# Optimization experiments

Hardware: AMD Instinct MI355X
Metric: run time of the kernel (lower is better)

## Reference

```python
import jax, jax.numpy as jnp
import numpy as np

EPS = 1e-8  # matches torch cosine_similarity eps


def setup_inputs() -> dict:
    key = jax.random.key(0)
    k1, k2 = jax.random.split(key)
    B, D = 8192, 128
    hid_positive = jax.random.normal(k1, (B, D), dtype=jnp.float32)
    hid_anchor = jax.random.normal(k2, (B, D), dtype=jnp.float32)
    return {"hid_positive": hid_positive, "hid_anchor": hid_anchor}


def reference(hid_positive, hid_anchor):
    # Original: anchor_batch = repeat_interleave(anchor, B) pairs every anchor i
    # with every positive j (positive[i] first per block, then the rest).
    # idx = +1 exactly on the (i, i) pairs, -1 elsewhere.
    # CosineEmbeddingLoss(margin=0, reduction='mean'):
    #   y=+1: 1 - cos ;  y=-1: max(0, cos)
    # Equivalent fused form: pairwise cosine matrix + masked loss, mean over B*B.
    a = hid_anchor / jnp.maximum(
        jnp.linalg.norm(hid_anchor, axis=1, keepdims=True), EPS)
    p = hid_positive / jnp.maximum(
        jnp.linalg.norm(hid_positive, axis=1, keepdims=True), EPS)
    cos = a @ p.T  # [B, B]; cos[i, j] = cos(anchor_i, positive_j)
    B = cos.shape[0]
    diag = jnp.eye(B, dtype=bool)
    loss = jnp.where(diag, 1.0 - cos, jnp.maximum(cos, 0.0))
    return jnp.mean(loss)
```

## Files before the change

### kernel.cpp

```cpp
#include <hip/hip_runtime.h>

typedef float f32x4 __attribute__((ext_vector_type(4)));
typedef int   i32x4 __attribute__((ext_vector_type(4)));
typedef int   i32x8 __attribute__((ext_vector_type(8)));

#define D 128
#define NBLK 256

__global__ void normalize_diag_kernel(const float* __restrict__ anc,
                                      const float* __restrict__ pos,
                                      unsigned char* __restrict__ wsA,
                                      unsigned char* __restrict__ wsP,
                                      float* __restrict__ diagP,
                                      int* __restrict__ counter) {
  if (blockIdx.x == 0 && threadIdx.x == 0)
    __hip_atomic_store(counter, 0, __ATOMIC_RELAXED, __HIP_MEMORY_SCOPE_AGENT);
  __shared__ float rowc[16];
  const int t = threadIdx.x;
  const int rl = t >> 4, l16 = t & 15;
  const int row = blockIdx.x * 16 + rl;
  const float* ar = anc + (size_t)row * D + l16 * 8;
  const float* pr = pos + (size_t)row * D + l16 * 8;
  float4 a0 = *(const float4*)ar, a1 = *(const float4*)(ar + 4);
  float4 p0 = *(const float4*)pr, p1 = *(const float4*)(pr + 4);
  float av[8] = {a0.x, a0.y, a0.z, a0.w, a1.x, a1.y, a1.z, a1.w};
  float pv[8] = {p0.x, p0.y, p0.z, p0.w, p1.x, p1.y, p1.z, p1.w};
  float ssa = 0.f, ssp = 0.f;
#pragma unroll
  for (int k = 0; k < 8; ++k) { ssa += av[k] * av[k]; ssp += pv[k] * pv[k]; }
#pragma unroll
  for (int off = 1; off < 16; off <<= 1) {
    ssa += __shfl_xor(ssa, off);
    ssp += __shfl_xor(ssp, off);
  }
  const float sa = 1.f / fmaxf(sqrtf(ssa), 1e-8f);
  const float sp = 1.f / fmaxf(sqrtf(ssp), 1e-8f);
  float an[8], pn[8];
  float dot = 0.f;
#pragma unroll
  for (int k = 0; k < 8; ++k) {
    an[k] = av[k] * sa;
    pn[k] = pv[k] * sp;
    dot += an[k] * pn[k];
  }
  int wa0 = __builtin_amdgcn_cvt_pk_fp8_f32(an[0], an[1], 0, false);
  wa0 = __builtin_amdgcn_cvt_pk_fp8_f32(an[2], an[3], wa0, true);
  int wa1 = __builtin_amdgcn_cvt_pk_fp8_f32(an[4], an[5], 0, false);
  wa1 = __builtin_amdgcn_cvt_pk_fp8_f32(an[6], an[7], wa1, true);
  int wp0 = __builtin_amdgcn_cvt_pk_fp8_f32(pn[0], pn[1], 0, false);
  wp0 = __builtin_amdgcn_cvt_pk_fp8_f32(pn[2], pn[3], wp0, true);
  int wp1 = __builtin_amdgcn_cvt_pk_fp8_f32(pn[4], pn[5], 0, false);
  wp1 = __builtin_amdgcn_cvt_pk_fp8_f32(pn[6], pn[7], wp1, true);
  *(int2*)(wsA + (size_t)row * D + l16 * 8) = make_int2(wa0, wa1);
  *(int2*)(wsP + (size_t)row * D + l16 * 8) = make_int2(wp0, wp1);
#pragma unroll
  for (int off = 1; off < 16; off <<= 1) dot += __shfl_xor(dot, off);
  if (l16 == 0) rowc[rl] = 1.f - dot - fmaxf(dot, 0.f);
  __syncthreads();
  if (t == 0) {
    float s = 0.f;
#pragma unroll
    for (int i = 0; i < 16; ++i) s += rowc[i];
    diagP[blockIdx.x] = s;
  }
}

__global__ __launch_bounds__(512, 2) void gemm_relu_sum_kernel(
    const unsigned char* __restrict__ wsA,
    const unsigned char* __restrict__ wsP,
    float* __restrict__ partials, const float* __restrict__ diagP,
    int* __restrict__ counter, float* __restrict__ out, float invBB) {
  __shared__ __align__(16) unsigned char ldsA[256 * 128];
  __shared__ __align__(16) unsigned char ldsB[4][128 * 128];
  __shared__ float wpart[8];
  __shared__ int lastFlag;
  const int tid = threadIdx.x;
  const int bid = blockIdx.x;
  const int w = tid >> 6, l = tid & 63;
  const int r16 = l & 15, kg = l >> 4;
  const int wrow = w >> 2, wcol = w & 3;
  const int rp = bid >> 3;
  const int cg = bid & 7;

  const unsigned char* gA = wsA + (size_t)rp * 256 * D;
  const unsigned char* gB = wsP + (size_t)(cg * 1024) * D;

#define STAGE_B(buf, tile)                                                     \
  {                                                                            \
    const unsigned char* gBt = gB + (size_t)(tile) * 128 * D;                  \
    char* lB = (char*)ldsB[buf];                                               \
    _Pragma("unroll") for (int it = 0; it < 2; ++it) {                         \
      const int g = it * 512 + tid;                                            \
      const int r = g >> 3, sl = g & 7;                                        \
      const int goff = r * 128 + ((sl ^ (r & 7)) * 16);                        \
      const int lbase = (it * 512 + w * 64) * 16;                              \
      __builtin_amdgcn_global_load_lds(                                        \
          (const __attribute__((address_space(1))) char*)(gBt + goff),         \
          (__attribute__((address_space(3))) char*)(lB + lbase), 16, 0, 0);    \
    }                                                                          \
  }

#pragma unroll
  for (int it = 0; it < 4; ++it) {
    const int g = it * 512 + tid;
    const int r = g >> 3, sl = g & 7;
    const int goff = r * 128 + ((sl ^ (r & 7)) * 16);
    const int lbase = (it * 512 + w * 64) * 16;
    __builtin_amdgcn_global_load_lds(
        (const __attribute__((address_space(1))) char*)(gA + goff),
        (__attribute__((address_space(3))) char*)((char*)ldsA + lbase), 16, 0, 0);
  }
  STAGE_B(0, 0)
  STAGE_B(1, 1)

  asm volatile("s_waitcnt vmcnt(4)" ::: "memory");
  __builtin_amdgcn_s_barrier();

  i32x8 af[8];
#pragma unroll
  for (int m = 0; m < 8; ++m) {
    const int r = wrow * 128 + m * 16 + r16;
    const unsigned char* base = (const unsigned char*)ldsA + r * 128;
    i32x4 lo = *(const i32x4*)(base + (((2 * kg) ^ (r & 7)) * 16));
    i32x4 hi = *(const i32x4*)(base + (((2 * kg + 1) ^ (r & 7)) * 16));
    af[m] = __builtin_shufflevector(lo, hi, 0, 1, 2, 3, 4, 5, 6, 7);
  }

  float s0 = 0.f, s1 = 0.f, s2 = 0.f, s3 = 0.f;
#pragma unroll
  for (int t = 0; t < 8; ++t) {
    if (t < 6) STAGE_B((t + 2) & 3, t + 2)
    if (t < 6)      asm volatile("s_waitcnt vmcnt(4)" ::: "memory");
    else if (t == 6) asm volatile("s_waitcnt vmcnt(2)" ::: "memory");
    else             asm volatile("s_waitcnt vmcnt(0)" ::: "memory");
    __builtin_amdgcn_s_barrier();

    const unsigned char* lB = (const unsigned char*)ldsB[t & 3];
    i32x8 bfr[2];
#pragma unroll
    for (int n = 0; n < 2; ++n) {
      const int r = wcol * 32 + n * 16 + r16;
      const unsigned char* base = lB + r * 128;
      i32x4 lo = *(const i32x4*)(base + (((2 * kg) ^ (r & 7)) * 16));
      i32x4 hi = *(const i32x4*)(base + (((2 * kg + 1) ^ (r & 7)) * 16));
      bfr[n] = __builtin_shufflevector(lo, hi, 0, 1, 2, 3, 4, 5, 6, 7);
    }

    f32x4 acc[8][2] = {};
    __builtin_amdgcn_s_setprio(1);
#pragma unroll
    for (int m = 0; m < 8; ++m)
#pragma unroll
      for (int n = 0; n < 2; ++n)
        acc[m][n] = __builtin_amdgcn_mfma_scale_f32_16x16x128_f8f6f4(
            af[m], bfr[n], acc[m][n], 0, 0,
            0, 0x7f7f7f7f, 0, 0x7f7f7f7f);
    __builtin_amdgcn_s_setprio(0);

#pragma unroll
    for (int m = 0; m < 8; ++m)
#pragma unroll
      for (int n = 0; n < 2; ++n) {
        s0 += fmaxf(acc[m][n][0], 0.f);
        s1 += fmaxf(acc[m][n][1], 0.f);
        s2 += fmaxf(acc[m][n][2], 0.f);
        s3 += fmaxf(acc[m][n][3], 0.f);
      }
  }

  float s = (s0 + s1) + (s2 + s3);
#pragma unroll
  for (int off = 32; off >= 1; off >>= 1) s += __shfl_xor(s, off);
  if (l == 0) wpart[w] = s;
  __syncthreads();
  if (tid == 0) {
    float b = 0.f;
#pragma unroll
    for (int i = 0; i < 8; ++i) b += wpart[i];
    __hip_atomic_store(&partials[bid], b, __ATOMIC_RELAXED,
                       __HIP_MEMORY_SCOPE_AGENT);
    __threadfence();
    const int ticket = __hip_atomic_fetch_add(counter, 1, __ATOMIC_ACQ_REL,
                                              __HIP_MEMORY_SCOPE_AGENT);
    lastFlag = (ticket == NBLK - 1) ? 1 : 0;
  }
  __syncthreads();

  if (lastFlag) {
    __threadfence();
    float v = diagP[tid];
    if (tid < NBLK)
      v += __hip_atomic_load(&partials[tid], __ATOMIC_RELAXED,
                             __HIP_MEMORY_SCOPE_AGENT);
#pragma unroll
    for (int off = 32; off >= 1; off >>= 1) v += __shfl_xor(v, off);
    if (l == 0) wpart[w] = v;
    __syncthreads();
    if (tid == 0) {
      float tot = 0.f;
#pragma unroll
      for (int i = 0; i < 8; ++i) tot += wpart[i];
      out[0] = tot * invBB;
    }
  }
#undef STAGE_B
}

extern "C" void kernel_launch(void* const* d_in, const int* in_sizes, int n_in,
                              void* d_out, int out_size, void* d_ws, size_t ws_size,
                              hipStream_t stream) {
  const float* pos = (const float*)d_in[0];
  const float* anc = (const float*)d_in[1];
  const int B = in_sizes[0] / D;

  char* ws = (char*)d_ws;
  unsigned char* wsA = (unsigned char*)ws;
  unsigned char* wsP = (unsigned char*)(ws + (size_t)B * D);
  float* partials = (float*)(ws + (size_t)2 * B * D);
  float* diagP = partials + NBLK;
  int* counter = (int*)(diagP + 512);

  const int nDiag = B / 16;
  const float invBB = 1.0f / ((float)B * (float)B);

  normalize_diag_kernel<<<nDiag, 256, 0, stream>>>(anc, pos, wsA, wsP, diagP,
                                                   counter);
  gemm_relu_sum_kernel<<<NBLK, 512, 0, stream>>>(wsA, wsP, partials, diagP,
                                                 counter, (float*)d_out, invBB);
}
```

Measured before the change: 31.39 us.

## Replace pipelined B-tile loop with one 256x128 tile per block over 2048 blocks

The GEMM kernel used 256 blocks of 512 threads, each looping over eight 128-column B tiles with a 4-deep global_load_lds pipeline. It now launches 2048 blocks of 256 threads, each computing a single 256x128 output tile with no inner loop, and raises occupancy to 3 blocks per CU. This removes the pipeline and barrier logic and spreads work over more blocks. In exchange, the A tile is reloaded 8x more often and each block stalls on its loads with no overlap. The final reduction now covers 2048 partials.

```diff
diff --git a/kernel.cpp b/kernel.cpp
--- a/kernel.cpp
+++ b/kernel.cpp
@@ -5,7 +5,7 @@
 typedef int   i32x8 __attribute__((ext_vector_type(8)));
 
 #define D 128
-#define NBLK 256
+#define GBLK 2048
 
 __global__ void normalize_diag_kernel(const float* __restrict__ anc,
                                       const float* __restrict__ pos,
@@ -65,56 +65,46 @@
   }
 }
 
-__global__ __launch_bounds__(512, 2) void gemm_relu_sum_kernel(
+__global__ __launch_bounds__(256, 3) void gemm_relu_sum_kernel(
     const unsigned char* __restrict__ wsA,
     const unsigned char* __restrict__ wsP,
     float* __restrict__ partials, const float* __restrict__ diagP,
     int* __restrict__ counter, float* __restrict__ out, float invBB) {
   __shared__ __align__(16) unsigned char ldsA[256 * 128];
-  __shared__ __align__(16) unsigned char ldsB[4][128 * 128];
-  __shared__ float wpart[8];
+  __shared__ __align__(16) unsigned char ldsB[128 * 128];
+  __shared__ float wpart[4];
   __shared__ int lastFlag;
   const int tid = threadIdx.x;
   const int bid = blockIdx.x;
   const int w = tid >> 6, l = tid & 63;
   const int r16 = l & 15, kg = l >> 4;
-  const int wrow = w >> 2, wcol = w & 3;
-  const int rp = bid >> 3;
-  const int cg = bid & 7;
+  const int wrow = w >> 1, wcol = w & 1;
+  const int rp = bid >> 6;
+  const int ct = bid & 63;
 
   const unsigned char* gA = wsA + (size_t)rp * 256 * D;
-  const unsigned char* gB = wsP + (size_t)(cg * 1024) * D;
-
-#define STAGE_B(buf, tile)                                                     \
-  {                                                                            \
-    const unsigned char* gBt = gB + (size_t)(tile) * 128 * D;                  \
-    char* lB = (char*)ldsB[buf];                                               \
-    _Pragma("unroll") for (int it = 0; it < 2; ++it) {                         \
-      const int g = it * 512 + tid;                                            \
-      const int r = g >> 3, sl = g & 7;                                        \
-      const int goff = r * 128 + ((sl ^ (r & 7)) * 16);                        \
-      const int lbase = (it * 512 + w * 64) * 16;                              \
-      __builtin_amdgcn_global_load_lds(                                        \
-          (const __attribute__((address_space(1))) char*)(gBt + goff),         \
-          (__attribute__((address_space(3))) char*)(lB + lbase), 16, 0, 0);    \
-    }                                                                          \
-  }
-
-#pragma unroll
-  for (int it = 0; it < 4; ++it) {
-    const int g = it * 512 + tid;
+  const unsigned char* gB = wsP + (size_t)ct * 128 * D;
+#pragma unroll
+  for (int it = 0; it < 8; ++it) {
+    const int g = it * 256 + tid;
     const int r = g >> 3, sl = g & 7;
     const int goff = r * 128 + ((sl ^ (r & 7)) * 16);
-    const int lbase = (it * 512 + w * 64) * 16;
+    const int lbase = (it * 256 + w * 64) * 16;
     __builtin_amdgcn_global_load_lds(
         (const __attribute__((address_space(1))) char*)(gA + goff),
         (__attribute__((address_space(3))) char*)((char*)ldsA + lbase), 16, 0, 0);
   }
-  STAGE_B(0, 0)
-  STAGE_B(1, 1)
-
-  asm volatile("s_waitcnt vmcnt(4)" ::: "memory");
-  __builtin_amdgcn_s_barrier();
+#pragma unroll
+  for (int it = 0; it < 4; ++it) {
+    const int g = it * 256 + tid;
+    const int r = g >> 3, sl = g & 7;
+    const int goff = r * 128 + ((sl ^ (r & 7)) * 16);
+    const int lbase = (it * 256 + w * 64) * 16;
+    __builtin_amdgcn_global_load_lds(
+        (const __attribute__((address_space(1))) char*)(gB + goff),
+        (__attribute__((address_space(3))) char*)((char*)ldsB + lbase), 16, 0, 0);
+  }
+  __syncthreads();
 
   i32x8 af[8];
 #pragma unroll
@@ -125,48 +115,37 @@
     i32x4 hi = *(const i32x4*)(base + (((2 * kg + 1) ^ (r & 7)) * 16));
     af[m] = __builtin_shufflevector(lo, hi, 0, 1, 2, 3, 4, 5, 6, 7);
   }
+  i32x8 bfr[4];
+#pragma unroll
+  for (int n = 0; n < 4; ++n) {
+    const int r = wcol * 64 + n * 16 + r16;
+    const unsigned char* base = (const unsigned char*)ldsB + r * 128;
+    i32x4 lo = *(const i32x4*)(base + (((2 * kg) ^ (r & 7)) * 16));
+    i32x4 hi = *(const i32x4*)(base + (((2 * kg + 1) ^ (r & 7)) * 16));
+    bfr[n] = __builtin_shufflevector(lo, hi, 0, 1, 2, 3, 4, 5, 6, 7);
+  }
+
+  f32x4 acc[8][4] = {};
+  __builtin_amdgcn_s_setprio(1);
+#pragma unroll
+  for (int m = 0; m < 8; ++m)
+#pragma unroll
+    for (int n = 0; n < 4; ++n)
+      acc[m][n] = __builtin_amdgcn_mfma_scale_f32_16x16x128_f8f6f4(
+          af[m], bfr[n], acc[m][n], 0, 0,
+          0, 0x7f7f7f7f, 0, 0x7f7f7f7f);
+  __builtin_amdgcn_s_setprio(0);
 
   float s0 = 0.f, s1 = 0.f, s2 = 0.f, s3 = 0.f;
 #pragma unroll
-  for (int t = 0; t < 8; ++t) {
-    if (t < 6) STAGE_B((t + 2) & 3, t + 2)
-    if (t < 6)      asm volatile("s_waitcnt vmcnt(4)" ::: "memory");
-    else if (t == 6) asm volatile("s_waitcnt vmcnt(2)" ::: "memory");
-    else             asm volatile("s_waitcnt vmcnt(0)" ::: "memory");
-    __builtin_amdgcn_s_barrier();
-
-    const unsigned char* lB = (const unsigned char*)ldsB[t & 3];
-    i32x8 bfr[2];
-#pragma unroll
-    for (int n = 0; n < 2; ++n) {
-      const int r = wcol * 32 + n * 16 + r16;
-      const unsigned char* base = lB + r * 128;
-      i32x4 lo = *(const i32x4*)(base + (((2 * kg) ^ (r & 7)) * 16));
-      i32x4 hi = *(const i32x4*)(base + (((2 * kg + 1) ^ (r & 7)) * 16));
-      bfr[n] = __builtin_shufflevector(lo, hi, 0, 1, 2, 3, 4, 5, 6, 7);
+  for (int m = 0; m < 8; ++m)
+#pragma unroll
+    for (int n = 0; n < 4; ++n) {
+      s0 += fmaxf(acc[m][n][0], 0.f);
+      s1 += fmaxf(acc[m][n][1], 0.f);
+      s2 += fmaxf(acc[m][n][2], 0.f);
+      s3 += fmaxf(acc[m][n][3], 0.f);
     }
-
-    f32x4 acc[8][2] = {};
-    __builtin_amdgcn_s_setprio(1);
-#pragma unroll
-    for (int m = 0; m < 8; ++m)
-#pragma unroll
-      for (int n = 0; n < 2; ++n)
-        acc[m][n] = __builtin_amdgcn_mfma_scale_f32_16x16x128_f8f6f4(
-            af[m], bfr[n], acc[m][n], 0, 0,
-            0, 0x7f7f7f7f, 0, 0x7f7f7f7f);
-    __builtin_amdgcn_s_setprio(0);
-
-#pragma unroll
-    for (int m = 0; m < 8; ++m)
-#pragma unroll
-      for (int n = 0; n < 2; ++n) {
-        s0 += fmaxf(acc[m][n][0], 0.f);
-        s1 += fmaxf(acc[m][n][1], 0.f);
-        s2 += fmaxf(acc[m][n][2], 0.f);
-        s3 += fmaxf(acc[m][n][3], 0.f);
-      }
-  }
 
   float s = (s0 + s1) + (s2 + s3);
 #pragma unroll
@@ -174,36 +153,30 @@
   if (l == 0) wpart[w] = s;
   __syncthreads();
   if (tid == 0) {
-    float b = 0.f;
-#pragma unroll
-    for (int i = 0; i < 8; ++i) b += wpart[i];
+    const float b = wpart[0] + wpart[1] + wpart[2] + wpart[3];
     __hip_atomic_store(&partials[bid], b, __ATOMIC_RELAXED,
                        __HIP_MEMORY_SCOPE_AGENT);
     __threadfence();
     const int ticket = __hip_atomic_fetch_add(counter, 1, __ATOMIC_ACQ_REL,
                                               __HIP_MEMORY_SCOPE_AGENT);
-    lastFlag = (ticket == NBLK - 1) ? 1 : 0;
+    lastFlag = (ticket == GBLK - 1) ? 1 : 0;
   }
   __syncthreads();
 
   if (lastFlag) {
     __threadfence();
-    float v = diagP[tid];
-    if (tid < NBLK)
-      v += __hip_atomic_load(&partials[tid], __ATOMIC_RELAXED,
+    float v = 0.f;
+    for (int i = tid; i < GBLK; i += 256)
+      v += __hip_atomic_load(&partials[i], __ATOMIC_RELAXED,
                              __HIP_MEMORY_SCOPE_AGENT);
+    for (int i = tid; i < 512; i += 256) v += diagP[i];
 #pragma unroll
     for (int off = 32; off >= 1; off >>= 1) v += __shfl_xor(v, off);
     if (l == 0) wpart[w] = v;
     __syncthreads();
-    if (tid == 0) {
-      float tot = 0.f;
-#pragma unroll
-      for (int i = 0; i < 8; ++i) tot += wpart[i];
-      out[0] = tot * invBB;
-    }
-  }
-#undef STAGE_B
+    if (tid == 0)
+      out[0] = (wpart[0] + wpart[1] + wpart[2] + wpart[3]) * invBB;
+  }
 }
 
 extern "C" void kernel_launch(void* const* d_in, const int* in_sizes, int n_in,
@@ -217,7 +190,7 @@
   unsigned char* wsA = (unsigned char*)ws;
   unsigned char* wsP = (unsigned char*)(ws + (size_t)B * D);
   float* partials = (float*)(ws + (size_t)2 * B * D);
-  float* diagP = partials + NBLK;
+  float* diagP = partials + GBLK;
   int* counter = (int*)(diagP + 512);
 
   const int nDiag = B / 16;
@@ -225,6 +198,6 @@
 
   normalize_diag_kernel<<<nDiag, 256, 0, stream>>>(anc, pos, wsA, wsP, diagP,
                                                    counter);
-  gemm_relu_sum_kernel<<<NBLK, 512, 0, stream>>>(wsA, wsP, partials, diagP,
+  gemm_relu_sum_kernel<<<GBLK, 256, 0, stream>>>(wsA, wsP, partials, diagP,
                                                  counter, (float*)d_out, invBB);
 }
```

Result: slower. 89.79 us (+186.0%).

## Use square 512x512 block tiles with all operands preloaded into LDS

Applied to the files above, without the earlier changes.

Each block now covers a 512x512 output tile instead of 256x1024. The full A and B panels (128 KB of FP8 in total) are loaded into LDS in a single upfront burst. This replaces the 4-deep pipelined B staging that used waitcnt and barriers, leaving one barrier before compute. The aim is less global traffic per block and less synchronisation, at the cost of no longer overlapping loads with MFMA work and needing far more LDS per block.

```diff
diff --git a/kernel.cpp b/kernel.cpp
--- a/kernel.cpp
+++ b/kernel.cpp
@@ -70,38 +70,22 @@
     const unsigned char* __restrict__ wsP,
     float* __restrict__ partials, const float* __restrict__ diagP,
     int* __restrict__ counter, float* __restrict__ out, float invBB) {
-  __shared__ __align__(16) unsigned char ldsA[256 * 128];
-  __shared__ __align__(16) unsigned char ldsB[4][128 * 128];
-  __shared__ float wpart[8];
-  __shared__ int lastFlag;
+  __shared__ __align__(16) unsigned char lds[131072];
+  unsigned char* ldsA = lds;
+  unsigned char* ldsB = lds + 65536;
+
   const int tid = threadIdx.x;
   const int bid = blockIdx.x;
   const int w = tid >> 6, l = tid & 63;
   const int r16 = l & 15, kg = l >> 4;
-  const int wrow = w >> 2, wcol = w & 3;
-  const int rp = bid >> 3;
-  const int cg = bid & 7;
-
-  const unsigned char* gA = wsA + (size_t)rp * 256 * D;
-  const unsigned char* gB = wsP + (size_t)(cg * 1024) * D;
-
-#define STAGE_B(buf, tile)                                                     \
-  {                                                                            \
-    const unsigned char* gBt = gB + (size_t)(tile) * 128 * D;                  \
-    char* lB = (char*)ldsB[buf];                                               \
-    _Pragma("unroll") for (int it = 0; it < 2; ++it) {                         \
-      const int g = it * 512 + tid;                                            \
-      const int r = g >> 3, sl = g & 7;                                        \
-      const int goff = r * 128 + ((sl ^ (r & 7)) * 16);                        \
-      const int lbase = (it * 512 + w * 64) * 16;                              \
-      __builtin_amdgcn_global_load_lds(                                        \
-          (const __attribute__((address_space(1))) char*)(gBt + goff),         \
-          (__attribute__((address_space(3))) char*)(lB + lbase), 16, 0, 0);    \
-    }                                                                          \
-  }
-
-#pragma unroll
-  for (int it = 0; it < 4; ++it) {
+  const int wrow = w >> 1, wcol = w & 1;
+  const int rp = bid >> 4;
+  const int cp = bid & 15;
+
+  const unsigned char* gA = wsA + (size_t)rp * 512 * D;
+  const unsigned char* gB = wsP + (size_t)cp * 512 * D;
+#pragma unroll
+  for (int it = 0; it < 8; ++it) {
     const int g = it * 512 + tid;
     const int r = g >> 3, sl = g & 7;
     const int goff = r * 128 + ((sl ^ (r & 7)) * 16);
@@ -109,18 +93,17 @@
     __builtin_amdgcn_global_load_lds(
         (const __attribute__((address_space(1))) char*)(gA + goff),
         (__attribute__((address_space(3))) char*)((char*)ldsA + lbase), 16, 0, 0);
-  }
-  STAGE_B(0, 0)
-  STAGE_B(1, 1)
-
-  asm volatile("s_waitcnt vmcnt(4)" ::: "memory");
-  __builtin_amdgcn_s_barrier();
+    __builtin_amdgcn_global_load_lds(
+        (const __attribute__((address_space(1))) char*)(gB + goff),
+        (__attribute__((address_space(3))) char*)((char*)ldsB + lbase), 16, 0, 0);
+  }
+  __syncthreads();
 
   i32x8 af[8];
 #pragma unroll
   for (int m = 0; m < 8; ++m) {
     const int r = wrow * 128 + m * 16 + r16;
-    const unsigned char* base = (const unsigned char*)ldsA + r * 128;
+    const unsigned char* base = ldsA + r * 128;
     i32x4 lo = *(const i32x4*)(base + (((2 * kg) ^ (r & 7)) * 16));
     i32x4 hi = *(const i32x4*)(base + (((2 * kg + 1) ^ (r & 7)) * 16));
     af[m] = __builtin_shufflevector(lo, hi, 0, 1, 2, 3, 4, 5, 6, 7);
@@ -128,24 +111,16 @@
 
   float s0 = 0.f, s1 = 0.f, s2 = 0.f, s3 = 0.f;
 #pragma unroll
-  for (int t = 0; t < 8; ++t) {
-    if (t < 6) STAGE_B((t + 2) & 3, t + 2)
-    if (t < 6)      asm volatile("s_waitcnt vmcnt(4)" ::: "memory");
-    else if (t == 6) asm volatile("s_waitcnt vmcnt(2)" ::: "memory");
-    else             asm volatile("s_waitcnt vmcnt(0)" ::: "memory");
-    __builtin_amdgcn_s_barrier();
-
-    const unsigned char* lB = (const unsigned char*)ldsB[t & 3];
+  for (int ct = 0; ct < 8; ++ct) {
     i32x8 bfr[2];
 #pragma unroll
     for (int n = 0; n < 2; ++n) {
-      const int r = wcol * 32 + n * 16 + r16;
-      const unsigned char* base = lB + r * 128;
+      const int r = wcol * 256 + ct * 32 + n * 16 + r16;
+      const unsigned char* base = ldsB + r * 128;
       i32x4 lo = *(const i32x4*)(base + (((2 * kg) ^ (r & 7)) * 16));
       i32x4 hi = *(const i32x4*)(base + (((2 * kg + 1) ^ (r & 7)) * 16));
       bfr[n] = __builtin_shufflevector(lo, hi, 0, 1, 2, 3, 4, 5, 6, 7);
     }
-
     f32x4 acc[8][2] = {};
     __builtin_amdgcn_s_setprio(1);
 #pragma unroll
@@ -156,7 +131,6 @@
             af[m], bfr[n], acc[m][n], 0, 0,
             0, 0x7f7f7f7f, 0, 0x7f7f7f7f);
     __builtin_amdgcn_s_setprio(0);
-
 #pragma unroll
     for (int m = 0; m < 8; ++m)
 #pragma unroll
@@ -168,6 +142,10 @@
       }
   }
 
+  __syncthreads();
+  float* wpart = (float*)lds;
+  int* lastFlag = (int*)(lds + 64);
+
   float s = (s0 + s1) + (s2 + s3);
 #pragma unroll
   for (int off = 32; off >= 1; off >>= 1) s += __shfl_xor(s, off);
@@ -182,11 +160,11 @@
     __threadfence();
     const int ticket = __hip_atomic_fetch_add(counter, 1, __ATOMIC_ACQ_REL,
                                               __HIP_MEMORY_SCOPE_AGENT);
-    lastFlag = (ticket == NBLK - 1) ? 1 : 0;
-  }
-  __syncthreads();
-
-  if (lastFlag) {
+    lastFlag[0] = (ticket == NBLK - 1) ? 1 : 0;
+  }
+  __syncthreads();
+
+  if (lastFlag[0]) {
     __threadfence();
     float v = diagP[tid];
     if (tid < NBLK)
@@ -203,7 +181,6 @@
       out[0] = tot * invBB;
     }
   }
-#undef STAGE_B
 }
 
 extern "C" void kernel_launch(void* const* d_in, const int* in_sizes, int n_in,
```

Result: faster. 30.53 us (-2.7%).
